# Optimization experiments

Measured on AMD Instinct MI355X. Metric: run time of the kernel, lower is better.

Reference implementation:

```python
import jax, jax.numpy as jnp
import numpy as np

N_NODES = 100000
N_EDGES = 1600000
N_GRAPHS = 64
IN_F, HID, OUT_F = 128, 256, 10


def setup_inputs() -> dict:
    key = jax.random.key(0)
    ks = jax.random.split(key, 9)
    x = jax.random.normal(ks[0], (N_NODES, IN_F), dtype=jnp.float32)
    edge_index = jax.random.randint(ks[1], (2, N_EDGES), 0, N_NODES, dtype=jnp.int64)
    batch = jnp.sort(jax.random.randint(ks[2], (N_NODES,), 0, N_GRAPHS, dtype=jnp.int64))
    # PyG GCNConv: lin (bias=False) weight [out, in], separate bias [out]
    def glorot(k, shape):
        lim = float(np.sqrt(6.0 / (shape[0] + shape[1])))
        return jax.random.uniform(k, shape, jnp.float32, -lim, lim)
    W1 = glorot(ks[3], (HID, IN_F));  b1 = jnp.zeros((HID,), jnp.float32)
    W2 = glorot(ks[4], (HID, HID));   b2 = jnp.zeros((HID,), jnp.float32)
    Wfc = glorot(ks[5], (OUT_F, HID))
    bfc = jax.random.uniform(ks[6], (OUT_F,), jnp.float32, -0.06, 0.06)
    return {"x": x, "edge_index": edge_index, "batch": batch,
            "W1": W1, "b1": b1, "W2": W2, "b2": b2, "Wfc": Wfc, "bfc": bfc}


def _gcn_norm(edge_index, n_nodes):
    # add self loops, compute symmetric normalization (PyG gcn_norm default)
    loop = jnp.arange(n_nodes, dtype=edge_index.dtype)
    src = jnp.concatenate([edge_index[0], loop])  # source j
    dst = jnp.concatenate([edge_index[1], loop])  # target i
    deg = jax.ops.segment_sum(jnp.ones_like(dst, jnp.float32), dst, num_segments=n_nodes)
    dinv = jnp.where(deg > 0, jax.lax.rsqrt(deg), 0.0)
    norm = dinv[src] * dinv[dst]  # [E+N]
    return src, dst, norm


def _gcn_conv(x, src, dst, norm, W, b, n_nodes):
    h = x @ W.T                                   # [N, out]
    msg = h[src] * norm[:, None]                  # gather + edge scale
    out = jax.ops.segment_sum(msg, dst, num_segments=n_nodes)  # scatter-add
    return out + b


def reference(x, edge_index, batch, W1, b1, W2, b2, Wfc, bfc):
    n = x.shape[0]
    src, dst, norm = _gcn_norm(edge_index, n)
    h = jax.nn.relu(_gcn_conv(x, src, dst, norm, W1, b1, n))
    h = jax.nn.relu(_gcn_conv(h, src, dst, norm, W2, b2, n))
    # global mean pool over graphs
    sums = jax.ops.segment_sum(h, batch, num_segments=N_GRAPHS)      # [G, HID]
    cnts = jax.ops.segment_sum(jnp.ones((n,), h.dtype), batch, num_segments=N_GRAPHS)
    pooled = sums / jnp.maximum(cnts, 1.0)[:, None]
    return pooled @ Wfc.T + bfc
```

## Files before the change

kernel.cpp:

```cpp
#include <hip/hip_runtime.h>

#define N_NODES 100000
#define N_EDGES 1600000
#define N_GRAPHS 64
#define IN_F 128
#define HID 256
#define OUT_F 10

#define SCAN_B 1024
#define SCAN_NB ((N_NODES + SCAN_B - 1) / SCAN_B)

typedef __attribute__((ext_vector_type(8))) short short8v;
typedef __attribute__((ext_vector_type(4))) float f32x4;

__device__ __forceinline__ unsigned short f2bf(float f) {
    unsigned int u = __float_as_uint(f);
    u += 0x7FFFu + ((u >> 16) & 1u);
    return (unsigned short)(u >> 16);
}
__device__ __forceinline__ float bf2f(unsigned short s) {
    return __uint_as_float((unsigned int)s << 16);
}

__global__ void k_count(const int* __restrict__ dst, int* __restrict__ cnt) {
    int e = blockIdx.x * blockDim.x + threadIdx.x;
    if (e < N_EDGES) atomicAdd(&cnt[dst[e]], 1);
}

__global__ void k_dinv(const int* __restrict__ cnt, float* __restrict__ dinv) {
    int i = blockIdx.x * blockDim.x + threadIdx.x;
    if (i < N_NODES) dinv[i] = rsqrtf((float)cnt[i] + 1.0f);
}

__global__ void k_tobf(const float* __restrict__ w, unsigned short* __restrict__ wb, int n8) {
    int t = blockIdx.x * blockDim.x + threadIdx.x;
    if (t >= n8) return;
    const float* p = w + (size_t)t * 8;
    float4 a = *(const float4*)p;
    float4 b = *(const float4*)(p + 4);
    unsigned int o0 = f2bf(a.x) | ((unsigned int)f2bf(a.y) << 16);
    unsigned int o1 = f2bf(a.z) | ((unsigned int)f2bf(a.w) << 16);
    unsigned int o2 = f2bf(b.x) | ((unsigned int)f2bf(b.y) << 16);
    unsigned int o3 = f2bf(b.z) | ((unsigned int)f2bf(b.w) << 16);
    *(uint4*)(wb + (size_t)t * 8) = make_uint4(o0, o1, o2, o3);
}

__global__ void k_xtobf(const float* __restrict__ x, const float* __restrict__ dinv,
                        unsigned short* __restrict__ xb) {
    int t = blockIdx.x * blockDim.x + threadIdx.x;
    if (t >= N_NODES * (IN_F / 8)) return;
    int node = t / (IN_F / 8);
    float sc = dinv[node];
    const float* p = x + (size_t)t * 8;
    float4 a = *(const float4*)p;
    float4 b = *(const float4*)(p + 4);
    unsigned int o0 = f2bf(a.x * sc) | ((unsigned int)f2bf(a.y * sc) << 16);
    unsigned int o1 = f2bf(a.z * sc) | ((unsigned int)f2bf(a.w * sc) << 16);
    unsigned int o2 = f2bf(b.x * sc) | ((unsigned int)f2bf(b.y * sc) << 16);
    unsigned int o3 = f2bf(b.z * sc) | ((unsigned int)f2bf(b.w * sc) << 16);
    *(uint4*)(xb + (size_t)t * 8) = make_uint4(o0, o1, o2, o3);
}

__global__ void k_scan1(const int* __restrict__ cnt, int* __restrict__ rowptr,
                        int* __restrict__ bsum) {
    __shared__ int sm[SCAN_B];
    int t = threadIdx.x, base = blockIdx.x * SCAN_B;
    int v = (base + t < N_NODES) ? cnt[base + t] : 0;
    int x = v;
    sm[t] = x;
    __syncthreads();
    for (int off = 1; off < SCAN_B; off <<= 1) {
        int add = (t >= off) ? sm[t - off] : 0;
        __syncthreads();
        x += add;
        sm[t] = x;
        __syncthreads();
    }
    if (base + t < N_NODES) rowptr[base + t] = x - v;
    if (t == SCAN_B - 1) bsum[blockIdx.x] = x;
}

__global__ void k_scan2(int* __restrict__ bsum) {
    __shared__ int sm[128];
    int t = threadIdx.x;
    int v = (t < SCAN_NB) ? bsum[t] : 0;
    int x = v;
    sm[t] = x;
    __syncthreads();
    for (int off = 1; off < 128; off <<= 1) {
        int add = (t >= off) ? sm[t - off] : 0;
        __syncthreads();
        x += add;
        sm[t] = x;
        __syncthreads();
    }
    if (t < SCAN_NB) bsum[t] = x - v;
}

__global__ void k_scan3(int* __restrict__ rowptr, const int* __restrict__ bsum) {
    int i = blockIdx.x * blockDim.x + threadIdx.x;
    if (i < N_NODES) rowptr[i] += bsum[i >> 10];
}

__global__ void k_fill(const int* __restrict__ src, const int* __restrict__ dst,
                       const int* __restrict__ rowptr, int* __restrict__ fill,
                       int* __restrict__ col) {
    int e = blockIdx.x * blockDim.x + threadIdx.x;
    if (e >= N_EDGES) return;
    int d = dst[e];
    int p = rowptr[d] + atomicAdd(&fill[d], 1);
    col[p] = src[e];
}

template<int W>
__global__ void __launch_bounds__(256)
k_aggv(const unsigned short* __restrict__ hb, const float* __restrict__ dinv,
       const int* __restrict__ rowptr, const int* __restrict__ cnt,
       const int* __restrict__ col, unsigned short* __restrict__ out) {
    constexpr int LR = W / 8;
    constexpr int NW = 64 / LR;
    int wid = threadIdx.x >> 6;
    int i = blockIdx.x * 4 + wid;
    if (i >= N_NODES) return;
    int lane = threadIdx.x & 63;
    int g = lane / LR;
    int s = lane % LR;
    float dd = dinv[i];
    int beg = rowptr[i] - 1;
    int total = cnt[i] + 1;
    float acc[8] = {};
    for (int v = 0; v < total; v += 2 * NW) {
        int iA = v + g, iB = v + NW + g;
        uint4 a = make_uint4(0u, 0u, 0u, 0u);
        uint4 b = make_uint4(0u, 0u, 0u, 0u);
        if (iA < total) {
            int r = (iA == 0) ? i : col[beg + iA];
            a = *(const uint4*)(hb + (size_t)r * W + s * 8);
        }
        if (iB < total) {
            int r = col[beg + iB];
            b = *(const uint4*)(hb + (size_t)r * W + s * 8);
        }
        acc[0] += bf2f((unsigned short)(a.x & 0xffffu));
        acc[1] += bf2f((unsigned short)(a.x >> 16));
        acc[2] += bf2f((unsigned short)(a.y & 0xffffu));
        acc[3] += bf2f((unsigned short)(a.y >> 16));
        acc[4] += bf2f((unsigned short)(a.z & 0xffffu));
        acc[5] += bf2f((unsigned short)(a.z >> 16));
        acc[6] += bf2f((unsigned short)(a.w & 0xffffu));
        acc[7] += bf2f((unsigned short)(a.w >> 16));
        acc[0] += bf2f((unsigned short)(b.x & 0xffffu));
        acc[1] += bf2f((unsigned short)(b.x >> 16));
        acc[2] += bf2f((unsigned short)(b.y & 0xffffu));
        acc[3] += bf2f((unsigned short)(b.y >> 16));
        acc[4] += bf2f((unsigned short)(b.z & 0xffffu));
        acc[5] += bf2f((unsigned short)(b.z >> 16));
        acc[6] += bf2f((unsigned short)(b.w & 0xffffu));
        acc[7] += bf2f((unsigned short)(b.w >> 16));
    }
    #pragma unroll
    for (int off = LR; off < 64; off <<= 1)
        #pragma unroll
        for (int c = 0; c < 8; ++c)
            acc[c] += __shfl_xor(acc[c], off, 64);
    if (g == 0) {
        unsigned int o0 = f2bf(dd * acc[0]) | ((unsigned int)f2bf(dd * acc[1]) << 16);
        unsigned int o1 = f2bf(dd * acc[2]) | ((unsigned int)f2bf(dd * acc[3]) << 16);
        unsigned int o2 = f2bf(dd * acc[4]) | ((unsigned int)f2bf(dd * acc[5]) << 16);
        unsigned int o3 = f2bf(dd * acc[6]) | ((unsigned int)f2bf(dd * acc[7]) << 16);
        *(uint4*)(out + (size_t)i * W + s * 8) = make_uint4(o0, o1, o2, o3);
    }
}

template<int K, bool FUSE>
__global__ void __launch_bounds__(256)
k_mgemm(const unsigned short* __restrict__ A, const unsigned short* __restrict__ Wb,
        const float* __restrict__ bias, unsigned short* __restrict__ Cb,
        const float* __restrict__ dinv, const int* __restrict__ batch,
        float* __restrict__ pooled) {
    constexpr int LDT = 72;
    __shared__ unsigned short Asl[128 * LDT];
    __shared__ unsigned short Bsl[128 * LDT];
    __shared__ float red[128];
    int row0 = blockIdx.x * 128;
    int col0 = blockIdx.y * 128;
    int t = threadIdx.x;
    int wid = t >> 6, lane = t & 63;
    int fr = lane & 15, fq = lane >> 4;
    int wr = wid >> 1, wc = wid & 1;

    f32x4 acc[4][4] = {};

    for (int kc = 0; kc < K; kc += 64) {
        #pragma unroll
        for (int p = 0; p < 4; ++p) {
            int idx = p * 256 + t;
            int r = idx >> 3;
            int c8 = (idx & 7) * 8;
            uint4 v = make_uint4(0u, 0u, 0u, 0u);
            int grow = row0 + r;
            if (grow < N_NODES) v = *(const uint4*)(A + (size_t)grow * K + kc + c8);
            *(uint4*)(Asl + r * LDT + c8) = v;
            uint4 w = *(const uint4*)(Wb + (size_t)(col0 + r) * K + kc + c8);
            *(uint4*)(Bsl + r * LDT + c8) = w;
        }
        __syncthreads();
        #pragma unroll
        for (int k0 = 0; k0 < 64; k0 += 32) {
            short8v af[4], bf[4];
            #pragma unroll
            for (int m = 0; m < 4; ++m)
                af[m] = *(const short8v*)(Asl + (wr * 64 + m * 16 + fr) * LDT + k0 + fq * 8);
            #pragma unroll
            for (int n = 0; n < 4; ++n)
                bf[n] = *(const short8v*)(Bsl + (wc * 64 + n * 16 + fr) * LDT + k0 + fq * 8);
            #pragma unroll
            for (int m = 0; m < 4; ++m)
                #pragma unroll
                for (int n = 0; n < 4; ++n)
                    acc[m][n] = __builtin_amdgcn_mfma_f32_16x16x32_bf16(af[m], bf[n], acc[m][n], 0, 0, 0);
        }
        __syncthreads();
    }

    float bv[4];
    #pragma unroll
    for (int n = 0; n < 4; ++n) bv[n] = bias[col0 + wc * 64 + n * 16 + fr];

    if (!FUSE) {
        #pragma unroll
        for (int m = 0; m < 4; ++m) {
            #pragma unroll
            for (int j = 0; j < 4; ++j) {
                int row = row0 + wr * 64 + m * 16 + fq * 4 + j;
                if (row >= N_NODES) continue;
                float sc = dinv[row];
                unsigned short* o = Cb + (size_t)row * HID + col0 + wc * 64;
                #pragma unroll
                for (int n = 0; n < 4; ++n) {
                    float v = fmaxf(acc[m][n][j] + bv[n], 0.f) * sc;
                    o[n * 16 + fr] = f2bf(v);
                }
            }
        }
    } else {
        int gm[4][4];
        #pragma unroll
        for (int m = 0; m < 4; ++m)
            #pragma unroll
            for (int j = 0; j < 4; ++j) {
                int row = row0 + wr * 64 + m * 16 + fq * 4 + j;
                gm[m][j] = (row < N_NODES) ? batch[row] : -1;
                #pragma unroll
                for (int n = 0; n < 4; ++n)
                    acc[m][n][j] = fmaxf(acc[m][n][j] + bv[n], 0.f);
            }
        int rhi = row0 + 127; if (rhi >= N_NODES) rhi = N_NODES - 1;
        int glo = batch[row0], ghi = batch[rhi];
        for (int g = glo; g <= ghi; ++g) {
            if (t < 128) red[t] = 0.f;
            __syncthreads();
            #pragma unroll
            for (int n = 0; n < 4; ++n) {
                float s = 0.f;
                #pragma unroll
                for (int m = 0; m < 4; ++m)
                    #pragma unroll
                    for (int j = 0; j < 4; ++j)
                        if (gm[m][j] == g) s += acc[m][n][j];
                if (s != 0.f) atomicAdd(&red[wc * 64 + n * 16 + fr], s);
            }
            __syncthreads();
            if (t < 128 && red[t] != 0.f)
                atomicAdd(&pooled[g * HID + col0 + t], red[t]);
            __syncthreads();
        }
    }
}

__global__ void k_cntg_bs(const int* __restrict__ batch, float* __restrict__ cntg) {
    int g = threadIdx.x;
    if (g >= N_GRAPHS) return;
    int lo = 0, hi = N_NODES;
    while (lo < hi) { int mid = (lo + hi) >> 1; if (batch[mid] < g) lo = mid + 1; else hi = mid; }
    int a = lo;
    lo = 0; hi = N_NODES;
    while (lo < hi) { int mid = (lo + hi) >> 1; if (batch[mid] < g + 1) lo = mid + 1; else hi = mid; }
    cntg[g] = (float)(lo - a);
}

__global__ void k_final(const float* __restrict__ pooled, const float* __restrict__ cntg,
                        const float* __restrict__ Wfc, const float* __restrict__ bfc,
                        float* __restrict__ out) {
    int t = blockIdx.x * blockDim.x + threadIdx.x;
    if (t >= N_GRAPHS * OUT_F) return;
    int g = t / OUT_F, o = t % OUT_F;
    float inv = 1.0f / fmaxf(cntg[g], 1.0f);
    float s = 0.f;
    for (int k = 0; k < HID; ++k) s += pooled[g * HID + k] * Wfc[o * HID + k];
    out[t] = s * inv + bfc[o];
}

extern "C" void kernel_launch(void* const* d_in, const int* in_sizes, int n_in,
                              void* d_out, int out_size, void* d_ws, size_t ws_size,
                              hipStream_t stream) {
    const float* x    = (const float*)d_in[0];
    const int*   ei   = (const int*)d_in[1];
    const int*   bat  = (const int*)d_in[2];
    const float* W1   = (const float*)d_in[3];
    const float* b1   = (const float*)d_in[4];
    const float* W2   = (const float*)d_in[5];
    const float* b2   = (const float*)d_in[6];
    const float* Wfc  = (const float*)d_in[7];
    const float* bfc  = (const float*)d_in[8];
    float* out = (float*)d_out;

    const int* src = ei;
    const int* dst = ei + N_EDGES;

    float* ws = (float*)d_ws;
    float* dinv    = ws + 0;
    float* pooled  = ws + 100096;
    float* cntg    = ws + 116480;
    int*   cnt     = (int*)(ws + 116608);
    int*   rowptr  = (int*)(ws + 216704);
    int*   fill    = (int*)(ws + 316928);
    int*   bsum    = (int*)(ws + 416928);
    int*   col     = (int*)(ws + 417056);
    unsigned short* W1b = (unsigned short*)(ws + 2017056);
    unsigned short* W2b = (unsigned short*)(ws + 2033440);
    unsigned short* xb  = (unsigned short*)(ws + 2066208);
    unsigned short* h1b = (unsigned short*)(ws + 8466208);
    unsigned short* aggb = (unsigned short*)(ws + 21266208);

    const int B = 256;

    hipMemsetAsync(pooled, 0, (16384 + 128) * 4, stream);
    hipMemsetAsync(cnt, 0, (size_t)(417056 - 116608) * 4, stream);

    k_count<<<(N_EDGES + B - 1) / B, B, 0, stream>>>(dst, cnt);
    k_dinv<<<(N_NODES + B - 1) / B, B, 0, stream>>>(cnt, dinv);
    k_tobf<<<(HID * IN_F / 8 + B - 1) / B, B, 0, stream>>>(W1, W1b, HID * IN_F / 8);
    k_tobf<<<(HID * HID / 8 + B - 1) / B, B, 0, stream>>>(W2, W2b, HID * HID / 8);
    k_xtobf<<<(N_NODES * (IN_F / 8) + B - 1) / B, B, 0, stream>>>(x, dinv, xb);
    k_scan1<<<SCAN_NB, SCAN_B, 0, stream>>>(cnt, rowptr, bsum);
    k_scan2<<<1, 128, 0, stream>>>(bsum);
    k_scan3<<<(N_NODES + B - 1) / B, B, 0, stream>>>(rowptr, bsum);
    k_fill<<<(N_EDGES + B - 1) / B, B, 0, stream>>>(src, dst, rowptr, fill, col);
    k_cntg_bs<<<1, 64, 0, stream>>>(bat, cntg);

    k_aggv<IN_F><<<(N_NODES + 3) / 4, 256, 0, stream>>>(xb, dinv, rowptr, cnt, col, aggb);
    {
        dim3 grid((N_NODES + 127) / 128, HID / 128);
        k_mgemm<IN_F, false><<<grid, 256, 0, stream>>>(aggb, W1b, b1, h1b, dinv, nullptr, nullptr);
    }

    k_aggv<HID><<<(N_NODES + 3) / 4, 256, 0, stream>>>(h1b, dinv, rowptr, cnt, col, aggb);
    {
        dim3 grid((N_NODES + 127) / 128, HID / 128);
        k_mgemm<HID, true><<<grid, 256, 0, stream>>>(aggb, W2b, b2, nullptr, nullptr, bat, pooled);
    }

    k_final<<<(N_GRAPHS * OUT_F + B - 1) / B, B, 0, stream>>>(pooled, cntg, Wfc, bfc, out);
}
```

Before: 482.4 us.

## Merge small setup kernels and unroll neighbor gathers four-wide in aggregation

Folds dinv into the first scan pass, merges the two weight-to-bf16 conversions into one launch, moves the per-graph count binary search into the final kernel, and merges the two memsets into one. The aggregation kernel now issues four independent row gathers per iteration instead of two, giving more memory requests in flight. This cuts launch count and latency overhead, at the cost of somewhat higher register pressure in the gather loop and redundant binary searches per output thread.

```diff
diff --git a/kernel.cpp b/kernel.cpp
--- a/kernel.cpp
+++ b/kernel.cpp
@@ -27,22 +27,21 @@
     if (e < N_EDGES) atomicAdd(&cnt[dst[e]], 1);
 }
 
-__global__ void k_dinv(const int* __restrict__ cnt, float* __restrict__ dinv) {
-    int i = blockIdx.x * blockDim.x + threadIdx.x;
-    if (i < N_NODES) dinv[i] = rsqrtf((float)cnt[i] + 1.0f);
-}
-
-__global__ void k_tobf(const float* __restrict__ w, unsigned short* __restrict__ wb, int n8) {
+__global__ void k_tobf2(const float* __restrict__ w1, unsigned short* __restrict__ w1b, int n1_8,
+                        const float* __restrict__ w2, unsigned short* __restrict__ w2b, int n2_8) {
     int t = blockIdx.x * blockDim.x + threadIdx.x;
-    if (t >= n8) return;
-    const float* p = w + (size_t)t * 8;
+    const float* p;
+    unsigned short* o;
+    if (t < n1_8) { p = w1 + (size_t)t * 8; o = w1b + (size_t)t * 8; }
+    else if (t < n1_8 + n2_8) { int u = t - n1_8; p = w2 + (size_t)u * 8; o = w2b + (size_t)u * 8; }
+    else return;
     float4 a = *(const float4*)p;
     float4 b = *(const float4*)(p + 4);
     unsigned int o0 = f2bf(a.x) | ((unsigned int)f2bf(a.y) << 16);
     unsigned int o1 = f2bf(a.z) | ((unsigned int)f2bf(a.w) << 16);
     unsigned int o2 = f2bf(b.x) | ((unsigned int)f2bf(b.y) << 16);
     unsigned int o3 = f2bf(b.z) | ((unsigned int)f2bf(b.w) << 16);
-    *(uint4*)(wb + (size_t)t * 8) = make_uint4(o0, o1, o2, o3);
+    *(uint4*)o = make_uint4(o0, o1, o2, o3);
 }
 
 __global__ void k_xtobf(const float* __restrict__ x, const float* __restrict__ dinv,
@@ -62,10 +61,11 @@
 }
 
 __global__ void k_scan1(const int* __restrict__ cnt, int* __restrict__ rowptr,
-                        int* __restrict__ bsum) {
+                        int* __restrict__ bsum, float* __restrict__ dinv) {
     __shared__ int sm[SCAN_B];
     int t = threadIdx.x, base = blockIdx.x * SCAN_B;
     int v = (base + t < N_NODES) ? cnt[base + t] : 0;
+    if (base + t < N_NODES) dinv[base + t] = rsqrtf((float)v + 1.0f);
     int x = v;
     sm[t] = x;
     __syncthreads();
@@ -112,7 +112,7 @@
     col[p] = src[e];
 }
 
-template<int W>
+template<int W, int U>
 __global__ void __launch_bounds__(256)
 k_aggv(const unsigned short* __restrict__ hb, const float* __restrict__ dinv,
        const int* __restrict__ rowptr, const int* __restrict__ cnt,
@@ -128,35 +128,30 @@
     float dd = dinv[i];
     int beg = rowptr[i] - 1;
     int total = cnt[i] + 1;
+    const unsigned short* hbs = hb + s * 8;
     float acc[8] = {};
-    for (int v = 0; v < total; v += 2 * NW) {
-        int iA = v + g, iB = v + NW + g;
-        uint4 a = make_uint4(0u, 0u, 0u, 0u);
-        uint4 b = make_uint4(0u, 0u, 0u, 0u);
-        if (iA < total) {
-            int r = (iA == 0) ? i : col[beg + iA];
-            a = *(const uint4*)(hb + (size_t)r * W + s * 8);
-        }
-        if (iB < total) {
-            int r = col[beg + iB];
-            b = *(const uint4*)(hb + (size_t)r * W + s * 8);
-        }
-        acc[0] += bf2f((unsigned short)(a.x & 0xffffu));
-        acc[1] += bf2f((unsigned short)(a.x >> 16));
-        acc[2] += bf2f((unsigned short)(a.y & 0xffffu));
-        acc[3] += bf2f((unsigned short)(a.y >> 16));
-        acc[4] += bf2f((unsigned short)(a.z & 0xffffu));
-        acc[5] += bf2f((unsigned short)(a.z >> 16));
-        acc[6] += bf2f((unsigned short)(a.w & 0xffffu));
-        acc[7] += bf2f((unsigned short)(a.w >> 16));
-        acc[0] += bf2f((unsigned short)(b.x & 0xffffu));
-        acc[1] += bf2f((unsigned short)(b.x >> 16));
-        acc[2] += bf2f((unsigned short)(b.y & 0xffffu));
-        acc[3] += bf2f((unsigned short)(b.y >> 16));
-        acc[4] += bf2f((unsigned short)(b.z & 0xffffu));
-        acc[5] += bf2f((unsigned short)(b.z >> 16));
-        acc[6] += bf2f((unsigned short)(b.w & 0xffffu));
-        acc[7] += bf2f((unsigned short)(b.w >> 16));
+    for (int v = 0; v < total; v += U * NW) {
+        uint4 d[U];
+        #pragma unroll
+        for (int u = 0; u < U; ++u) {
+            int idx = v + u * NW + g;
+            d[u] = make_uint4(0u, 0u, 0u, 0u);
+            if (idx < total) {
+                int r = (idx == 0) ? i : col[beg + idx];
+                d[u] = *(const uint4*)(hbs + (size_t)r * W);
+            }
+        }
+        #pragma unroll
+        for (int u = 0; u < U; ++u) {
+            acc[0] += bf2f((unsigned short)(d[u].x & 0xffffu));
+            acc[1] += bf2f((unsigned short)(d[u].x >> 16));
+            acc[2] += bf2f((unsigned short)(d[u].y & 0xffffu));
+            acc[3] += bf2f((unsigned short)(d[u].y >> 16));
+            acc[4] += bf2f((unsigned short)(d[u].z & 0xffffu));
+            acc[5] += bf2f((unsigned short)(d[u].z >> 16));
+            acc[6] += bf2f((unsigned short)(d[u].w & 0xffffu));
+            acc[7] += bf2f((unsigned short)(d[u].w >> 16));
+        }
     }
     #pragma unroll
     for (int off = LR; off < 64; off <<= 1)
@@ -278,24 +273,18 @@
     }
 }
 
-__global__ void k_cntg_bs(const int* __restrict__ batch, float* __restrict__ cntg) {
-    int g = threadIdx.x;
-    if (g >= N_GRAPHS) return;
+__global__ void k_final(const float* __restrict__ pooled, const int* __restrict__ batch,
+                        const float* __restrict__ Wfc, const float* __restrict__ bfc,
+                        float* __restrict__ out) {
+    int t = blockIdx.x * blockDim.x + threadIdx.x;
+    if (t >= N_GRAPHS * OUT_F) return;
+    int g = t / OUT_F, o = t % OUT_F;
     int lo = 0, hi = N_NODES;
     while (lo < hi) { int mid = (lo + hi) >> 1; if (batch[mid] < g) lo = mid + 1; else hi = mid; }
     int a = lo;
     lo = 0; hi = N_NODES;
     while (lo < hi) { int mid = (lo + hi) >> 1; if (batch[mid] < g + 1) lo = mid + 1; else hi = mid; }
-    cntg[g] = (float)(lo - a);
-}
-
-__global__ void k_final(const float* __restrict__ pooled, const float* __restrict__ cntg,
-                        const float* __restrict__ Wfc, const float* __restrict__ bfc,
-                        float* __restrict__ out) {
-    int t = blockIdx.x * blockDim.x + threadIdx.x;
-    if (t >= N_GRAPHS * OUT_F) return;
-    int g = t / OUT_F, o = t % OUT_F;
-    float inv = 1.0f / fmaxf(cntg[g], 1.0f);
+    float inv = 1.0f / fmaxf((float)(lo - a), 1.0f);
     float s = 0.f;
     for (int k = 0; k < HID; ++k) s += pooled[g * HID + k] * Wfc[o * HID + k];
     out[t] = s * inv + bfc[o];
@@ -332,34 +321,32 @@
     unsigned short* xb  = (unsigned short*)(ws + 2066208);
     unsigned short* h1b = (unsigned short*)(ws + 8466208);
     unsigned short* aggb = (unsigned short*)(ws + 21266208);
+    (void)cntg;
 
     const int B = 256;
 
-    hipMemsetAsync(pooled, 0, (16384 + 128) * 4, stream);
-    hipMemsetAsync(cnt, 0, (size_t)(417056 - 116608) * 4, stream);
+    hipMemsetAsync(pooled, 0, (size_t)(417056 - 100096) * 4, stream);
 
     k_count<<<(N_EDGES + B - 1) / B, B, 0, stream>>>(dst, cnt);
-    k_dinv<<<(N_NODES + B - 1) / B, B, 0, stream>>>(cnt, dinv);
-    k_tobf<<<(HID * IN_F / 8 + B - 1) / B, B, 0, stream>>>(W1, W1b, HID * IN_F / 8);
-    k_tobf<<<(HID * HID / 8 + B - 1) / B, B, 0, stream>>>(W2, W2b, HID * HID / 8);
-    k_xtobf<<<(N_NODES * (IN_F / 8) + B - 1) / B, B, 0, stream>>>(x, dinv, xb);
-    k_scan1<<<SCAN_NB, SCAN_B, 0, stream>>>(cnt, rowptr, bsum);
+    k_scan1<<<SCAN_NB, SCAN_B, 0, stream>>>(cnt, rowptr, bsum, dinv);
     k_scan2<<<1, 128, 0, stream>>>(bsum);
     k_scan3<<<(N_NODES + B - 1) / B, B, 0, stream>>>(rowptr, bsum);
+    k_tobf2<<<((HID * IN_F + HID * HID) / 8 + B - 1) / B, B, 0, stream>>>(
+        W1, W1b, HID * IN_F / 8, W2, W2b, HID * HID / 8);
+    k_xtobf<<<(N_NODES * (IN_F / 8) + B - 1) / B, B, 0, stream>>>(x, dinv, xb);
     k_fill<<<(N_EDGES + B - 1) / B, B, 0, stream>>>(src, dst, rowptr, fill, col);
-    k_cntg_bs<<<1, 64, 0, stream>>>(bat, cntg);
-
-    k_aggv<IN_F><<<(N_NODES + 3) / 4, 256, 0, stream>>>(xb, dinv, rowptr, cnt, col, aggb);
+
+    k_aggv<IN_F, 4><<<(N_NODES + 3) / 4, 256, 0, stream>>>(xb, dinv, rowptr, cnt, col, aggb);
     {
         dim3 grid((N_NODES + 127) / 128, HID / 128);
         k_mgemm<IN_F, false><<<grid, 256, 0, stream>>>(aggb, W1b, b1, h1b, dinv, nullptr, nullptr);
     }
 
-    k_aggv<HID><<<(N_NODES + 3) / 4, 256, 0, stream>>>(h1b, dinv, rowptr, cnt, col, aggb);
+    k_aggv<HID, 4><<<(N_NODES + 3) / 4, 256, 0, stream>>>(h1b, dinv, rowptr, cnt, col, aggb);
     {
         dim3 grid((N_NODES + 127) / 128, HID / 128);
         k_mgemm<HID, true><<<grid, 256, 0, stream>>>(aggb, W2b, b2, nullptr, nullptr, bat, pooled);
     }
 
-    k_final<<<(N_GRAPHS * OUT_F + B - 1) / B, B, 0, stream>>>(pooled, cntg, Wfc, bfc, out);
-}
+    k_final<<<(N_GRAPHS * OUT_F + B - 1) / B, B, 0, stream>>>(pooled, bat, Wfc, bfc, out);
+}
```

New measurement: 470.1 us. 2.6% less time.
